# Optimization experiments

Hardware: AMD Instinct MI355X
Metric: run time of the kernel (lower is better)

The kernel has to match this reference:

```python
import jax, jax.numpy as jnp
import numpy as np

H = 256      # hidden_size
L = 20       # max_length
V = 29       # output_size (vocab)
LAT = H + 8


def setup_inputs() -> dict:
    key = jax.random.key(0)
    ks = jax.random.split(key, 20)
    s = 0.05
    return {
        "input_tensor": jax.random.randint(ks[0], (1,), 0, V),
        "hidden": jax.random.normal(ks[1], (1, 1, H), dtype=jnp.float32),
        "encoder_outputs": jax.random.normal(ks[2], (L, H), dtype=jnp.float32),
        "cond": jax.random.randint(ks[3], (2,), 0, 4),
        "is_head": 1,
        # parameters (PyTorch Linear convention: weight [out, in])
        "emb": jax.random.normal(ks[4], (V, H), dtype=jnp.float32) * s,
        "w_l2d": jax.random.normal(ks[5], (H, LAT), dtype=jnp.float32) * s,
        "b_l2d": jnp.zeros((H,), dtype=jnp.float32),
        "w_attn": jax.random.normal(ks[6], (L, 2 * H), dtype=jnp.float32) * s,
        "b_attn": jnp.zeros((L,), dtype=jnp.float32),
        "w_comb": jax.random.normal(ks[7], (H, 2 * H), dtype=jnp.float32) * s,
        "b_comb": jnp.zeros((H,), dtype=jnp.float32),
        "w_ih": jax.random.normal(ks[8], (3 * H, H), dtype=jnp.float32) * s,
        "w_hh": jax.random.normal(ks[9], (3 * H, H), dtype=jnp.float32) * s,
        "b_ih": jnp.zeros((3 * H,), dtype=jnp.float32),
        "b_hh": jnp.zeros((3 * H,), dtype=jnp.float32),
        "w_out": jax.random.normal(ks[10], (V, H), dtype=jnp.float32) * s,
        "b_out": jnp.zeros((V,), dtype=jnp.float32),
    }


def gru_cell(x, h, w_ih, w_hh, b_ih, b_hh):
    # x, h: [1, H]; PyTorch GRU gate order: r, z, n
    gi = x @ w_ih.T + b_ih
    gh = h @ w_hh.T + b_hh
    ir, iz, inn = jnp.split(gi, 3, axis=-1)
    hr, hz, hn = jnp.split(gh, 3, axis=-1)
    r = jax.nn.sigmoid(ir + hr)
    z = jax.nn.sigmoid(iz + hz)
    n = jnp.tanh(inn + r * hn)
    return (1.0 - z) * n + z * h


def reference(input_tensor, hidden, encoder_outputs, cond, is_head,
              emb, w_l2d, b_l2d, w_attn, b_attn, w_comb, b_comb,
              w_ih, w_hh, b_ih, b_hh, w_out, b_out):
    if is_head:
        c = jnp.concatenate([jax.nn.one_hot(cond[0], 4),
                             jax.nn.one_hot(cond[1], 4)]).astype(hidden.dtype)  # [8]
        hidden = jnp.concatenate([hidden, c[None, None, :]], axis=2)  # [1,1,H+8]
        hidden = hidden @ w_l2d.T + b_l2d                              # [1,1,H]
    embedded = emb[input_tensor].reshape(1, 1, -1)                     # [1,1,H] (dropout: eval mode)
    attn_in = jnp.concatenate([embedded[0], hidden[0]], axis=1)        # [1,2H]
    attn_weights = jax.nn.softmax(attn_in @ w_attn.T + b_attn, axis=1) # [1,L]
    attn_applied = attn_weights @ encoder_outputs                      # [1,H]
    output = jnp.concatenate([embedded[0], attn_applied], axis=1)      # [1,2H]
    output = jax.nn.relu(output @ w_comb.T + b_comb)                   # [1,H]
    h_new = gru_cell(output, hidden[0], w_ih, w_hh, b_ih, b_hh)        # [1,H]
    logits = jax.nn.log_softmax(h_new @ w_out.T + b_out, axis=1)       # [1,V]
    return logits, h_new[None], attn_weights
```

## Files before the change

### kernel.cpp

```cpp
#include <hip/hip_runtime.h>

#define H 256
#define L 20
#define V 29
#define LAT 264
#define NBLK 97
#define NTHR 256
#define PZN 0xAAAAAAAAu


typedef __attribute__((address_space(3))) unsigned int lds_u32;
typedef __attribute__((address_space(1))) unsigned int glb_u32;

__device__ __forceinline__ void g2l(const float* g, float* l, int lane) {
    __builtin_amdgcn_global_load_lds(
        (glb_u32*)(unsigned long long)(g + 4 * lane),
        (lds_u32*)l, 16, 0, 0);
}

__device__ __forceinline__ float wsum(float v) {
#pragma unroll
    for (int o = 32; o > 0; o >>= 1) v += __shfl_xor(v, o, 64);
    return v;
}

__device__ __forceinline__ float wmax(float v) {
#pragma unroll
    for (int o = 32; o > 0; o >>= 1) v = fmaxf(v, __shfl_xor(v, o, 64));
    return v;
}

__device__ __forceinline__ float dot44(float4 a, float4 b) {
    return a.x * b.x + a.y * b.y + a.z * b.z + a.w * b.w;
}

__device__ __forceinline__ float dot4(float4 a, float b0, float b1, float b2, float b3) {
    return a.x * b0 + a.y * b1 + a.z * b2 + a.w * b3;
}

__device__ __forceinline__ void stws(float* p, float v) {
    __hip_atomic_store(p, v, __ATOMIC_RELAXED, __HIP_MEMORY_SCOPE_AGENT);
}

__device__ __forceinline__ float pollf(const float* p) {
    union { unsigned u; float f; } v;
    long spins = 0;
    for (;;) {
        v.u = __hip_atomic_load((const unsigned*)p, __ATOMIC_RELAXED,
                                __HIP_MEMORY_SCOPE_AGENT);
        if (v.u != PZN) break;
        __builtin_amdgcn_s_sleep(1);
        if (++spins > 5000000L) break;
    }
    return v.f;
}

__global__ __launch_bounds__(NTHR) void decoder_step(
    const int* inp, const float* hidden, const float* enc,
    const int* cond, const int* is_head,
    const float* emb, const float* w_l2d, const float* b_l2d,
    const float* w_attn, const float* b_attn,
    const float* w_comb, const float* b_comb,
    const float* w_ih, const float* w_hh,
    const float* b_ih, const float* b_hh,
    const float* w_out, const float* b_out,
    float* ws, float* out)
{
    extern __shared__ float sm[];
    const int b = blockIdx.x;
    const int t = threadIdx.x;
    const int wave = t >> 6, lane = t & 63;

    if (b < 32) {
        const int c0 = b * 8;
        if (is_head[0]) {
            const float4 x4 = ((const float4*)hidden)[lane];
            float xt = 0.f;
            if (lane < 8) {
                int c = (lane < 4) ? cond[0] : cond[1];
                xt = (c == (lane & 3)) ? 1.f : 0.f;
            }
#pragma unroll
            for (int q = 0; q < 2; ++q) {
                int r = c0 + wave * 2 + q;
                const float* wr = w_l2d + r * LAT;
                float4 w4 = ((const float4*)wr)[lane];
                float s = dot44(w4, x4);
                if (lane < 8) s += wr[256 + lane] * xt;
                s = wsum(s);
                if (lane == 0) stws(&ws[r], s + b_l2d[r]);
            }
        } else {
            if (t < 8) stws(&ws[c0 + t], hidden[c0 + t]);
        }

    } else if (b < 64) {
        const int k = b - 32, r0 = k * 8;
        float* encl = sm;
        float* wah  = sm + 5120;
        float* wcl  = sm + 10240;
        float* lg   = sm + 14336;

#pragma unroll
        for (int i = 0; i < 5; ++i) {
            int r = wave * 5 + i;
            g2l(enc + r * H, encl + r * H, lane);
            g2l(w_attn + r * 2 * H + H, wah + r * H, lane);
        }
#pragma unroll
        for (int q = 0; q < 2; ++q) {
            int cr = wave * 2 + q;
            const float* src = w_comb + (r0 + cr) * 2 * H;
            g2l(src,     wcl + cr * 2 * H,     lane);
            g2l(src + H, wcl + cr * 2 * H + H, lane);
        }

        const float* erow = emb + inp[0] * H;
        const float4 e4 = ((const float4*)erow)[lane];
        float bcq[2];
#pragma unroll
        for (int q = 0; q < 2; ++q) bcq[q] = b_comb[r0 + wave * 2 + q];
        float lge[5];
#pragma unroll
        for (int i = 0; i < 5; ++i) {
            int r = wave * 5 + i;
            float4 w4 = ((const float4*)(w_attn + r * 2 * H))[lane];
            lge[i] = wsum(dot44(w4, e4)) + b_attn[r];
        }

        float h0 = pollf(ws + 4 * lane);
        float h1 = pollf(ws + 4 * lane + 1);
        float h2 = pollf(ws + 4 * lane + 2);
        float h3 = pollf(ws + 4 * lane + 3);
        asm volatile("s_waitcnt vmcnt(0)" ::: "memory");

#pragma unroll
        for (int i = 0; i < 5; ++i) {
            int r = wave * 5 + i;
            float4 w4 = ((const float4*)(wah + r * H))[lane];
            float s = wsum(dot4(w4, h0, h1, h2, h3));
            if (lane == 0) lg[r] = lge[i] + s;
        }
        __syncthreads();

        float v = (lane < L) ? lg[lane] : -1e30f;
        float m = wmax(v);
        float e = (lane < L) ? __expf(v - m) : 0.f;
        float inv = 1.f / wsum(e);
        if (k == 0 && wave == 0 && lane < L) out[V + H + lane] = e * inv;

        float4 app = make_float4(0.f, 0.f, 0.f, 0.f);
#pragma unroll
        for (int l = 0; l < L; ++l) {
            float a = __shfl(e, l, 64) * inv;
            float4 ev = ((const float4*)(encl + l * H))[lane];
            app.x += a * ev.x; app.y += a * ev.y;
            app.z += a * ev.z; app.w += a * ev.w;
        }

#pragma unroll
        for (int q = 0; q < 2; ++q) {
            int cr = wave * 2 + q;
            float4 wa = ((const float4*)(wcl + cr * 2 * H))[lane];
            float4 wb = ((const float4*)(wcl + cr * 2 * H + H))[lane];
            float s = wsum(dot44(wa, e4) + dot44(wb, app));
            if (lane == 0) stws(&ws[512 + r0 + cr], fmaxf(s + bcq[q], 0.f));
        }

    } else if (b < 96) {
        const int k = b - 64, c0 = k * 8;
        float* wh  = sm;
        float* wi  = sm + 6144;
        float* ghs = sm + 12288;
        float* gis = sm + 12320;
        float* xh  = sm + 12352;

#pragma unroll
        for (int i = 0; i < 6; ++i) {
            int mm = wave * 6 + i;
            int g = mm >> 3, rr = c0 + (mm & 7);
            g2l(w_hh + (g * H + rr) * H, wh + mm * H, lane);
            g2l(w_ih + (g * H + rr) * H, wi + mm * H, lane);
        }
        float bh[6], bi[6];
#pragma unroll
        for (int i = 0; i < 6; ++i) {
            int mm = wave * 6 + i;
            int g = mm >> 3;
            bh[i] = b_hh[g * H + c0 + (mm & 7)];
            bi[i] = b_ih[g * H + c0 + (mm & 7)];
        }

        float h0 = pollf(ws + 4 * lane);
        float h1 = pollf(ws + 4 * lane + 1);
        float h2 = pollf(ws + 4 * lane + 2);
        float h3 = pollf(ws + 4 * lane + 3);
        if (wave == 0) ((float4*)xh)[lane] = make_float4(h0, h1, h2, h3);
        asm volatile("s_waitcnt vmcnt(0)" ::: "memory");

#pragma unroll
        for (int i = 0; i < 6; ++i) {
            int mm = wave * 6 + i;
            float4 w4 = ((const float4*)(wh + mm * H))[lane];
            float s = wsum(dot4(w4, h0, h1, h2, h3));
            if (lane == 0) ghs[mm] = s + bh[i];
        }

        float o0 = pollf(ws + 512 + 4 * lane);
        float o1 = pollf(ws + 512 + 4 * lane + 1);
        float o2 = pollf(ws + 512 + 4 * lane + 2);
        float o3 = pollf(ws + 512 + 4 * lane + 3);

#pragma unroll
        for (int i = 0; i < 6; ++i) {
            int mm = wave * 6 + i;
            float4 w4 = ((const float4*)(wi + mm * H))[lane];
            float s = wsum(dot4(w4, o0, o1, o2, o3));
            if (lane == 0) gis[mm] = s + bi[i];
        }
        __syncthreads();

        if (t < 8) {
            float r = 1.f / (1.f + __expf(-(gis[t] + ghs[t])));
            float z = 1.f / (1.f + __expf(-(gis[8 + t] + ghs[8 + t])));
            float n = tanhf(gis[16 + t] + r * ghs[16 + t]);
            float h = (1.f - z) * n + z * xh[c0 + t];
            out[V + c0 + t] = h;
            stws(&ws[768 + c0 + t], h);
        }

    } else {
        float* wo = sm;
        float* lg = sm + 7424;
        for (int r = wave; r < V; r += 4)
            g2l(w_out + r * H, wo + r * H, lane);
        float bo = (lane < V) ? b_out[lane] : 0.f;

        float n0 = pollf(ws + 768 + 4 * lane);
        float n1 = pollf(ws + 768 + 4 * lane + 1);
        float n2 = pollf(ws + 768 + 4 * lane + 2);
        float n3 = pollf(ws + 768 + 4 * lane + 3);
        asm volatile("s_waitcnt vmcnt(0)" ::: "memory");

        for (int r = wave; r < V; r += 4) {
            float4 w4 = ((const float4*)(wo + r * H))[lane];
            float s = wsum(dot4(w4, n0, n1, n2, n3));
            if (lane == 0) lg[r] = s;
        }
        __syncthreads();
        if (wave == 0) {
            float v = (lane < V) ? lg[lane] + bo : -1e30f;
            float m = wmax(v);
            float e = (lane < V) ? __expf(v - m) : 0.f;
            float s2 = wsum(e);
            float ls = logf(s2);
            if (lane < V) out[lane] = v - m - ls;
        }
    }
}

extern "C" void kernel_launch(void* const* d_in, const int* in_sizes, int n_in,
                              void* d_out, int out_size, void* d_ws, size_t ws_size,
                              hipStream_t stream) {
    const int* inp      = (const int*)d_in[0];
    const float* hidden = (const float*)d_in[1];
    const float* enc    = (const float*)d_in[2];
    const int* cond     = (const int*)d_in[3];
    const int* is_head  = (const int*)d_in[4];
    const float* emb    = (const float*)d_in[5];
    const float* w_l2d  = (const float*)d_in[6];
    const float* b_l2d  = (const float*)d_in[7];
    const float* w_attn = (const float*)d_in[8];
    const float* b_attn = (const float*)d_in[9];
    const float* w_comb = (const float*)d_in[10];
    const float* b_comb = (const float*)d_in[11];
    const float* w_ih   = (const float*)d_in[12];
    const float* w_hh   = (const float*)d_in[13];
    const float* b_ih   = (const float*)d_in[14];
    const float* b_hh   = (const float*)d_in[15];
    const float* w_out  = (const float*)d_in[16];
    const float* b_out  = (const float*)d_in[17];

    float* ws = (float*)d_ws;
    float* out = (float*)d_out;

    const size_t smem = 14368 * sizeof(float);
    decoder_step<<<NBLK, NTHR, smem, stream>>>(
        inp, hidden, enc, cond, is_head, emb, w_l2d, b_l2d, w_attn, b_attn,
        w_comb, b_comb, w_ih, w_hh, b_ih, b_hh, w_out, b_out, ws, out);
}
```

Baseline: 104.0 us.

## Recompute latent-to-hidden projection redundantly per block instead of cross-block polling

Removes the 32 blocks that computed the latent2decoder projection and published it through workspace polling. Each attention/combine block and each GRU block now computes the full 256-row projection locally into shared memory, which drops one inter-block dependency stage and shrinks the grid to 65 blocks. In exchange every block reads the whole w_l2d matrix (about 270KB) and does 64 wave reductions per wave, a large redundant load that could cost more than the polling latency it removes.

```diff
diff --git a/kernel.cpp b/kernel.cpp
--- a/kernel.cpp
+++ b/kernel.cpp
@@ -4,7 +4,7 @@
 #define L 20
 #define V 29
 #define LAT 264
-#define NBLK 97
+#define NBLK 65
 #define NTHR 256
 #define PZN 0xAAAAAAAAu
 
@@ -32,10 +32,6 @@
 
 __device__ __forceinline__ float dot44(float4 a, float4 b) {
     return a.x * b.x + a.y * b.y + a.z * b.z + a.w * b.w;
-}
-
-__device__ __forceinline__ float dot4(float4 a, float b0, float b1, float b2, float b3) {
-    return a.x * b0 + a.y * b1 + a.z * b2 + a.w * b3;
 }
 
 __device__ __forceinline__ void stws(float* p, float v) {
@@ -53,6 +49,32 @@
         if (++spins > 5000000L) break;
     }
     return v.f;
+}
+
+__device__ __forceinline__ void hidden2_local(
+    float* h2, const float* hidden, const float* w_l2d, const float* b_l2d,
+    const int* cond, const int* is_head, int t, int wave, int lane)
+{
+    if (is_head[0]) {
+        const float4 x4 = ((const float4*)hidden)[lane];
+        float xt = 0.f;
+        if (lane < 8) {
+            int c = (lane < 4) ? cond[0] : cond[1];
+            xt = (c == (lane & 3)) ? 1.f : 0.f;
+        }
+#pragma unroll 4
+        for (int i = 0; i < 64; ++i) {
+            int r = wave * 64 + i;
+            const float* wr = w_l2d + r * LAT;
+            float4 w4 = ((const float4*)wr)[lane];
+            float s = dot44(w4, x4);
+            if (lane < 8) s += wr[256 + lane] * xt;
+            s = wsum(s);
+            if (lane == 0) h2[r] = s + b_l2d[r];
+        }
+    } else {
+        h2[t] = hidden[t];
+    }
 }
 
 __global__ __launch_bounds__(NTHR) void decoder_step(
@@ -72,34 +94,12 @@
     const int wave = t >> 6, lane = t & 63;
 
     if (b < 32) {
-        const int c0 = b * 8;
-        if (is_head[0]) {
-            const float4 x4 = ((const float4*)hidden)[lane];
-            float xt = 0.f;
-            if (lane < 8) {
-                int c = (lane < 4) ? cond[0] : cond[1];
-                xt = (c == (lane & 3)) ? 1.f : 0.f;
-            }
-#pragma unroll
-            for (int q = 0; q < 2; ++q) {
-                int r = c0 + wave * 2 + q;
-                const float* wr = w_l2d + r * LAT;
-                float4 w4 = ((const float4*)wr)[lane];
-                float s = dot44(w4, x4);
-                if (lane < 8) s += wr[256 + lane] * xt;
-                s = wsum(s);
-                if (lane == 0) stws(&ws[r], s + b_l2d[r]);
-            }
-        } else {
-            if (t < 8) stws(&ws[c0 + t], hidden[c0 + t]);
-        }
-
-    } else if (b < 64) {
-        const int k = b - 32, r0 = k * 8;
+        const int k = b, r0 = k * 8;
         float* encl = sm;
         float* wah  = sm + 5120;
         float* wcl  = sm + 10240;
-        float* lg   = sm + 14336;
+        float* h2   = sm + 14336;
+        float* lg   = sm + 14592;
 
 #pragma unroll
         for (int i = 0; i < 5; ++i) {
@@ -128,17 +128,16 @@
             lge[i] = wsum(dot44(w4, e4)) + b_attn[r];
         }
 
-        float h0 = pollf(ws + 4 * lane);
-        float h1 = pollf(ws + 4 * lane + 1);
-        float h2 = pollf(ws + 4 * lane + 2);
-        float h3 = pollf(ws + 4 * lane + 3);
+        hidden2_local(h2, hidden, w_l2d, b_l2d, cond, is_head, t, wave, lane);
         asm volatile("s_waitcnt vmcnt(0)" ::: "memory");
-
+        __syncthreads();
+
+        const float4 hv = ((const float4*)h2)[lane];
 #pragma unroll
         for (int i = 0; i < 5; ++i) {
             int r = wave * 5 + i;
             float4 w4 = ((const float4*)(wah + r * H))[lane];
-            float s = wsum(dot4(w4, h0, h1, h2, h3));
+            float s = wsum(dot44(w4, hv));
             if (lane == 0) lg[r] = lge[i] + s;
         }
         __syncthreads();
@@ -167,13 +166,13 @@
             if (lane == 0) stws(&ws[512 + r0 + cr], fmaxf(s + bcq[q], 0.f));
         }
 
-    } else if (b < 96) {
-        const int k = b - 64, c0 = k * 8;
+    } else if (b < 64) {
+        const int k = b - 32, c0 = k * 8;
         float* wh  = sm;
         float* wi  = sm + 6144;
-        float* ghs = sm + 12288;
-        float* gis = sm + 12320;
-        float* xh  = sm + 12352;
+        float* xh  = sm + 12288;
+        float* ghs = sm + 12544;
+        float* gis = sm + 12576;
 
 #pragma unroll
         for (int i = 0; i < 6; ++i) {
@@ -191,18 +190,16 @@
             bi[i] = b_ih[g * H + c0 + (mm & 7)];
         }
 
-        float h0 = pollf(ws + 4 * lane);
-        float h1 = pollf(ws + 4 * lane + 1);
-        float h2 = pollf(ws + 4 * lane + 2);
-        float h3 = pollf(ws + 4 * lane + 3);
-        if (wave == 0) ((float4*)xh)[lane] = make_float4(h0, h1, h2, h3);
+        hidden2_local(xh, hidden, w_l2d, b_l2d, cond, is_head, t, wave, lane);
         asm volatile("s_waitcnt vmcnt(0)" ::: "memory");
-
+        __syncthreads();
+
+        const float4 hv = ((const float4*)xh)[lane];
 #pragma unroll
         for (int i = 0; i < 6; ++i) {
             int mm = wave * 6 + i;
             float4 w4 = ((const float4*)(wh + mm * H))[lane];
-            float s = wsum(dot4(w4, h0, h1, h2, h3));
+            float s = wsum(dot44(w4, hv));
             if (lane == 0) ghs[mm] = s + bh[i];
         }
 
@@ -210,12 +207,13 @@
         float o1 = pollf(ws + 512 + 4 * lane + 1);
         float o2 = pollf(ws + 512 + 4 * lane + 2);
         float o3 = pollf(ws + 512 + 4 * lane + 3);
+        const float4 ov = make_float4(o0, o1, o2, o3);
 
 #pragma unroll
         for (int i = 0; i < 6; ++i) {
             int mm = wave * 6 + i;
             float4 w4 = ((const float4*)(wi + mm * H))[lane];
-            float s = wsum(dot4(w4, o0, o1, o2, o3));
+            float s = wsum(dot44(w4, ov));
             if (lane == 0) gis[mm] = s + bi[i];
         }
         __syncthreads();
@@ -240,11 +238,12 @@
         float n1 = pollf(ws + 768 + 4 * lane + 1);
         float n2 = pollf(ws + 768 + 4 * lane + 2);
         float n3 = pollf(ws + 768 + 4 * lane + 3);
+        const float4 nv = make_float4(n0, n1, n2, n3);
         asm volatile("s_waitcnt vmcnt(0)" ::: "memory");
 
         for (int r = wave; r < V; r += 4) {
             float4 w4 = ((const float4*)(wo + r * H))[lane];
-            float s = wsum(dot4(w4, n0, n1, n2, n3));
+            float s = wsum(dot44(w4, nv));
             if (lane == 0) lg[r] = s;
         }
         __syncthreads();
@@ -284,7 +283,7 @@
     float* ws = (float*)d_ws;
     float* out = (float*)d_out;
 
-    const size_t smem = 14368 * sizeof(float);
+    const size_t smem = 14624 * sizeof(float);
     decoder_step<<<NBLK, NTHR, smem, stream>>>(
         inp, hidden, enc, cond, is_head, emb, w_l2d, b_l2d, w_attn, b_attn,
         w_comb, b_comb, w_ih, w_hh, b_ih, b_hh, w_out, b_out, ws, out);
```

New measurement: 140.6 us. +35.1%, slower.
